# Performance work log

Hardware: AMD Instinct MI355X
Metric: run time of the kernel (lower is better)

The kernel has to match this reference:

```python
import jax, jax.numpy as jnp
import numpy as np

B, C, H, W = 8, 256, 128, 128
HEADS, DIM_HEAD = 4, 32
HID = HEADS * DIM_HEAD  # 128


def setup_inputs() -> dict:
    key = jax.random.key(0)
    k1, k2, k3, k4 = jax.random.split(key, 4)
    x = jax.random.normal(k1, (B, C, H, W), dtype=jnp.float32)
    # 1x1 conv weights stored as [out_ch, in_ch]
    w_qkv = jax.random.normal(k2, (3 * HID, C), dtype=jnp.float32) * (1.0 / np.sqrt(C))
    w_out = jax.random.normal(k3, (C, HID), dtype=jnp.float32) * (1.0 / np.sqrt(HID))
    b_out = jax.random.normal(k4, (C,), dtype=jnp.float32) * 0.01
    return {"x": x, "w_qkv": w_qkv, "w_out": w_out, "b_out": b_out}


def reference(x, w_qkv, w_out, b_out):
    b, c, h, w = x.shape
    n = h * w
    # 1x1 conv == channel matmul
    qkv = jnp.einsum('oc,bchw->bohw', w_qkv, x)  # [b, 3*HID, h, w]
    q, k, v = jnp.split(qkv, 3, axis=1)
    # rearrange 'b (heads d) h w -> b heads d (h w)'
    def to_heads(t):
        return t.reshape(b, HEADS, DIM_HEAD, n)
    q, k, v = to_heads(q), to_heads(k), to_heads(v)
    k = jax.nn.softmax(k, axis=-1)  # over spatial n
    # q_scale is False: q used as-is
    context = jnp.einsum('bhdn,bhen->bhde', k, v)   # [b, heads, d, e] small
    out = jnp.einsum('bhde,bhdn->bhen', context, q)  # [b, heads, e, n]
    out = out.reshape(b, HID, h, w)
    out = jnp.einsum('oc,bchw->bohw', w_out, out) + b_out[None, :, None, None]
    return out
```

## Files before the change

kernel.cpp:

```cpp
#include <hip/hip_runtime.h>
#include <stdint.h>

#define BB 8
#define CIN 256
#define NSP 16384
#define HID 128

typedef __bf16 bfrag __attribute__((ext_vector_type(8)));
typedef float  f32x4 __attribute__((ext_vector_type(4)));

__device__ __forceinline__ unsigned short f2bf(float f) {
  union { float f; unsigned int u; } v; v.f = f;
  unsigned int u = v.u;
  return (unsigned short)((u + 0x7FFFu + ((u >> 16) & 1u)) >> 16);
}

__global__ __launch_bounds__(256) void la_prep(const float* __restrict__ w_qkv,
                                               unsigned short* __restrict__ wkvb) {
  const int blk = blockIdx.x;
  const int t = threadIdx.x;
  const int off = (blk * 256 + t) * 4;
  const float4 wv4 = *(const float4*)(w_qkv + (size_t)128 * CIN + off);
  ushort4 p;
  p.x = f2bf(wv4.x); p.y = f2bf(wv4.y); p.z = f2bf(wv4.z); p.w = f2bf(wv4.w);
  *(ushort4*)(wkvb + off) = p;
}

__global__ __launch_bounds__(512, 4) void la_fused(const float* __restrict__ x,
                                                   const unsigned short* __restrict__ wkvb,
                                                   float* __restrict__ ctxp,
                                                   float* __restrict__ sumsp) {
  __shared__ __align__(16) union {
    struct { unsigned short Xb[2][128][40]; } g;
    struct { unsigned short Lk[64][140]; unsigned short Lv[64][140];
             float Pc[4][1024]; } e;
  } sh;
  const int chunk = blockIdx.x;
  const int n0 = chunk * 128;
  const int b = blockIdx.y;
  const int t = threadIdx.x;
  const int lane = t & 63, wv = t >> 6;
  const int l15 = lane & 15, q = lane >> 4;
  const int cl = t & 31;
  const int n16 = (t >> 5) * 8;
  const float* xp = x + (size_t)b * CIN * NSP + n0;
  f32x4 acc[2][8];
#pragma unroll
  for (int i = 0; i < 2; ++i)
#pragma unroll
    for (int j = 0; j < 8; ++j) acc[i][j] = 0.0f;

  float4 xa0, xa1;
  {
    const float* xr = xp + (size_t)cl * NSP + n16;
    xa0 = *(const float4*)xr;
    xa1 = *(const float4*)(xr + 4);
  }
  {
    sh.g.Xb[0][n16 + 0][cl] = f2bf(xa0.x);
    sh.g.Xb[0][n16 + 1][cl] = f2bf(xa0.y);
    sh.g.Xb[0][n16 + 2][cl] = f2bf(xa0.z);
    sh.g.Xb[0][n16 + 3][cl] = f2bf(xa0.w);
    sh.g.Xb[0][n16 + 4][cl] = f2bf(xa1.x);
    sh.g.Xb[0][n16 + 5][cl] = f2bf(xa1.y);
    sh.g.Xb[0][n16 + 6][cl] = f2bf(xa1.z);
    sh.g.Xb[0][n16 + 7][cl] = f2bf(xa1.w);
    const float* xr = xp + (size_t)(32 + cl) * NSP + n16;
    xa0 = *(const float4*)xr;
    xa1 = *(const float4*)(xr + 4);
  }
  __syncthreads();

#pragma unroll
  for (int kc = 0; kc < 8; ++kc) {
    const int p = kc & 1;
    bfrag a0 = *(const bfrag*)(wkvb + (size_t)(wv * 16 + l15) * CIN + kc * 32 + q * 8);
    bfrag a1 = *(const bfrag*)(wkvb + (size_t)(128 + wv * 16 + l15) * CIN + kc * 32 + q * 8);
    if (kc < 7) {
      sh.g.Xb[p ^ 1][n16 + 0][cl] = f2bf(xa0.x);
      sh.g.Xb[p ^ 1][n16 + 1][cl] = f2bf(xa0.y);
      sh.g.Xb[p ^ 1][n16 + 2][cl] = f2bf(xa0.z);
      sh.g.Xb[p ^ 1][n16 + 3][cl] = f2bf(xa0.w);
      sh.g.Xb[p ^ 1][n16 + 4][cl] = f2bf(xa1.x);
      sh.g.Xb[p ^ 1][n16 + 5][cl] = f2bf(xa1.y);
      sh.g.Xb[p ^ 1][n16 + 6][cl] = f2bf(xa1.z);
      sh.g.Xb[p ^ 1][n16 + 7][cl] = f2bf(xa1.w);
      if (kc < 6) {
        const float* xr = xp + (size_t)((kc + 2) * 32 + cl) * NSP + n16;
        xa0 = *(const float4*)xr;
        xa1 = *(const float4*)(xr + 4);
      }
    }
#pragma unroll
    for (int ni = 0; ni < 8; ++ni) {
      bfrag bbv = *(const bfrag*)&sh.g.Xb[p][ni * 16 + l15][q * 8];
      acc[0][ni] = __builtin_amdgcn_mfma_f32_16x16x32_bf16(a0, bbv, acc[0][ni], 0, 0, 0);
      acc[1][ni] = __builtin_amdgcn_mfma_f32_16x16x32_bf16(a1, bbv, acc[1][ni], 0, 0, 0);
    }
    __syncthreads();
  }

#pragma unroll
  for (int ni = 0; ni < 8; ++ni)
#pragma unroll
    for (int rg = 0; rg < 4; ++rg) acc[0][ni][rg] = __expf(acc[0][ni][rg]);

  {
    float sp[4] = {0.f, 0.f, 0.f, 0.f};
#pragma unroll
    for (int ni = 0; ni < 8; ++ni)
#pragma unroll
      for (int rg = 0; rg < 4; ++rg) sp[rg] += acc[0][ni][rg];
#pragma unroll
    for (int rg = 0; rg < 4; ++rg) {
      float s = sp[rg];
      s += __shfl_down(s, 8, 16);
      s += __shfl_down(s, 4, 16);
      s += __shfl_down(s, 2, 16);
      s += __shfl_down(s, 1, 16);
      if (l15 == 0)
        sumsp[((size_t)b * 128 + chunk) * 128 + wv * 16 + q * 4 + rg] = s;
    }
  }
  float* cp = ctxp + ((size_t)b * 128 + chunk) * 4096;
#pragma unroll
  for (int ph = 0; ph < 2; ++ph) {
    if ((wv >> 2) == ph) {
      const int r = (wv & 3) * 16 + q * 4;
#pragma unroll
      for (int ni = 0; ni < 8; ++ni)
#pragma unroll
        for (int rg = 0; rg < 4; ++rg) {
          sh.e.Lk[r + rg][ni * 16 + l15] = f2bf(acc[0][ni][rg]);
          sh.e.Lv[r + rg][ni * 16 + l15] = f2bf(acc[1][ni][rg]);
        }
    }
    __syncthreads();
    const int hl = wv >> 2, nq = wv & 3;
    f32x4 c2[2][2];
    c2[0][0] = 0.f; c2[0][1] = 0.f; c2[1][0] = 0.f; c2[1][1] = 0.f;
    bfrag ka[2], vb[2];
#pragma unroll
    for (int d2 = 0; d2 < 2; ++d2)
      ka[d2] = *(const bfrag*)&sh.e.Lk[hl * 32 + d2 * 16 + l15][nq * 32 + q * 8];
#pragma unroll
    for (int e2 = 0; e2 < 2; ++e2)
      vb[e2] = *(const bfrag*)&sh.e.Lv[hl * 32 + e2 * 16 + l15][nq * 32 + q * 8];
#pragma unroll
    for (int d2 = 0; d2 < 2; ++d2)
#pragma unroll
      for (int e2 = 0; e2 < 2; ++e2)
        c2[d2][e2] = __builtin_amdgcn_mfma_f32_16x16x32_bf16(ka[d2], vb[e2], c2[d2][e2], 0, 0, 0);
    const int slot = hl * 2 + (nq & 1);
    if (nq < 2) {
#pragma unroll
      for (int d2 = 0; d2 < 2; ++d2)
#pragma unroll
        for (int e2 = 0; e2 < 2; ++e2)
#pragma unroll
          for (int rg = 0; rg < 4; ++rg)
            sh.e.Pc[slot][(d2 * 16 + q * 4 + rg) * 32 + e2 * 16 + l15] = c2[d2][e2][rg];
    }
    __syncthreads();
    if (nq >= 2) {
#pragma unroll
      for (int d2 = 0; d2 < 2; ++d2)
#pragma unroll
        for (int e2 = 0; e2 < 2; ++e2)
#pragma unroll
          for (int rg = 0; rg < 4; ++rg)
            sh.e.Pc[slot][(d2 * 16 + q * 4 + rg) * 32 + e2 * 16 + l15] += c2[d2][e2][rg];
    }
    __syncthreads();
    for (int idx = t; idx < 2048; idx += 512) {
      const int h2 = idx >> 10, pos = idx & 1023;
      cp[(ph * 2 + h2) * 1024 + pos] = sh.e.Pc[h2 * 2][pos] + sh.e.Pc[h2 * 2 + 1][pos];
    }
    __syncthreads();
  }
}

__global__ __launch_bounds__(256) void la_reduce(const float* __restrict__ ctxp,
                                                 const float* __restrict__ sumsp,
                                                 float* __restrict__ ctxu,
                                                 float* __restrict__ sums) {
  const int blk = blockIdx.x;
  const int t = threadIdx.x;
  if (blk < 128) {
    const int gid = blk * 256 + t;
    const int b = gid >> 12, pos = gid & 4095;
    const float* base = ctxp + (size_t)b * 128 * 4096 + pos;
    float s = 0.f;
#pragma unroll 8
    for (int c = 0; c < 128; ++c) s += base[(size_t)c * 4096];
    ctxu[gid] = s;
  } else {
    const int gid = (blk - 128) * 256 + t;
    const int b = gid >> 7, row = gid & 127;
    const float* base = sumsp + (size_t)b * 128 * 128 + row;
    float s = 0.f;
#pragma unroll 8
    for (int c = 0; c < 128; ++c) s += base[c * 128];
    sums[gid] = s;
  }
}

__global__ __launch_bounds__(256) void la_mid(const float* __restrict__ w_out,
                                              const float* __restrict__ ctxu,
                                              const float* __restrict__ sums,
                                              const float* __restrict__ w_qkv,
                                              unsigned short* __restrict__ wcomb) {
  __shared__ float wrow[128];
  const int o = blockIdx.x;
  const int b = blockIdx.y;
  const int t = threadIdx.x;
  if (t < 128) {
    const int h = t >> 5, d = t & 31;
    const float* wr = w_out + (size_t)o * HID + h * 32;
    const float* cr = ctxu + ((size_t)(b * 4 + h) * 32 + d) * 32;
    float s = 0.f;
#pragma unroll 8
    for (int e = 0; e < 32; ++e) s += wr[e] * cr[e];
    wrow[t] = s * (1.0f / sums[b * 128 + t]);
  }
  __syncthreads();
  float s = 0.f;
#pragma unroll 8
  for (int hd = 0; hd < 128; ++hd) s += wrow[hd] * w_qkv[(size_t)hd * CIN + t];
  wcomb[((size_t)b * 256 + o) * 256 + t] = f2bf(s);
}

__global__ __launch_bounds__(512, 4) void la_out(const unsigned short* __restrict__ wcomb,
                                                 const float* __restrict__ x,
                                                 const float* __restrict__ b_out,
                                                 float* __restrict__ out) {
  __shared__ __align__(16) unsigned short Bt[2][128][40];
  const int n0 = blockIdx.x * 128;
  const int b = blockIdx.y;
  const int t = threadIdx.x;
  const int lane = t & 63, wv = t >> 6;
  const int l15 = lane & 15, q = lane >> 4;
  const int wm = (wv & 3) * 64;
  const int wn = (wv >> 2) * 64;
  const int cl = t & 31, n16 = (t >> 5) * 8;
  const float* xp = x + (size_t)b * CIN * NSP + n0;
  const unsigned short* abase = wcomb + (size_t)b * 256 * 256;
  f32x4 acc[4][4];
#pragma unroll
  for (int i = 0; i < 4; ++i)
#pragma unroll
    for (int j = 0; j < 4; ++j) acc[i][j] = 0.0f;

  float4 xa0, xa1;
  {
    const float* xr = xp + (size_t)cl * NSP + n16;
    xa0 = *(const float4*)xr;
    xa1 = *(const float4*)(xr + 4);
  }
  {
    Bt[0][n16 + 0][cl] = f2bf(xa0.x);
    Bt[0][n16 + 1][cl] = f2bf(xa0.y);
    Bt[0][n16 + 2][cl] = f2bf(xa0.z);
    Bt[0][n16 + 3][cl] = f2bf(xa0.w);
    Bt[0][n16 + 4][cl] = f2bf(xa1.x);
    Bt[0][n16 + 5][cl] = f2bf(xa1.y);
    Bt[0][n16 + 6][cl] = f2bf(xa1.z);
    Bt[0][n16 + 7][cl] = f2bf(xa1.w);
    const float* xr = xp + (size_t)(32 + cl) * NSP + n16;
    xa0 = *(const float4*)xr;
    xa1 = *(const float4*)(xr + 4);
  }
  __syncthreads();

#pragma unroll
  for (int kc = 0; kc < 8; ++kc) {
    const int p = kc & 1;
    bfrag a[4];
#pragma unroll
    for (int mi = 0; mi < 4; ++mi)
      a[mi] = *(const bfrag*)(abase + (size_t)(wm + mi * 16 + l15) * 256 + kc * 32 + q * 8);
    if (kc < 7) {
      Bt[p ^ 1][n16 + 0][cl] = f2bf(xa0.x);
      Bt[p ^ 1][n16 + 1][cl] = f2bf(xa0.y);
      Bt[p ^ 1][n16 + 2][cl] = f2bf(xa0.z);
      Bt[p ^ 1][n16 + 3][cl] = f2bf(xa0.w);
      Bt[p ^ 1][n16 + 4][cl] = f2bf(xa1.x);
      Bt[p ^ 1][n16 + 5][cl] = f2bf(xa1.y);
      Bt[p ^ 1][n16 + 6][cl] = f2bf(xa1.z);
      Bt[p ^ 1][n16 + 7][cl] = f2bf(xa1.w);
      if (kc < 6) {
        const float* xr = xp + (size_t)((kc + 2) * 32 + cl) * NSP + n16;
        xa0 = *(const float4*)xr;
        xa1 = *(const float4*)(xr + 4);
      }
    }
#pragma unroll
    for (int ni = 0; ni < 4; ++ni) {
      bfrag bbv = *(const bfrag*)&Bt[p][wn + ni * 16 + l15][q * 8];
#pragma unroll
      for (int mi = 0; mi < 4; ++mi)
        acc[mi][ni] = __builtin_amdgcn_mfma_f32_16x16x32_bf16(a[mi], bbv, acc[mi][ni], 0, 0, 0);
    }
    __syncthreads();
  }
  float* obase = out + (size_t)b * 256 * NSP;
#pragma unroll
  for (int mi = 0; mi < 4; ++mi) {
    const int ob = wm + mi * 16 + q * 4;
    const float4 bias = *(const float4*)(b_out + ob);
    float ba[4] = {bias.x, bias.y, bias.z, bias.w};
#pragma unroll
    for (int ni = 0; ni < 4; ++ni) {
      const int n = n0 + wn + ni * 16 + l15;
#pragma unroll
      for (int rg = 0; rg < 4; ++rg)
        obase[(size_t)(ob + rg) * NSP + n] = acc[mi][ni][rg] + ba[rg];
    }
  }
}


extern "C" void kernel_launch(void* const* d_in, const int* in_sizes, int n_in,
                              void* d_out, int out_size, void* d_ws, size_t ws_size,
                              hipStream_t stream) {
  (void)in_sizes; (void)n_in; (void)out_size; (void)ws_size;
  const float* x     = (const float*)d_in[0];
  const float* w_qkv = (const float*)d_in[1];
  const float* w_out = (const float*)d_in[2];
  const float* b_out = (const float*)d_in[3];
  float* out = (float*)d_out;
  char* ws = (char*)d_ws;
  unsigned short* wkvb  = (unsigned short*)(ws);
  float* ctxp           = (float*)(ws + 131072);
  float* sumsp          = (float*)(ws + 16908288);
  float* ctxu           = (float*)(ws + 17432576);
  float* sums           = (float*)(ws + 17563648);
  unsigned short* wcomb = (unsigned short*)(ws + 17567744);

  la_prep<<<dim3(64), dim3(256), 0, stream>>>(w_qkv, wkvb);
  la_fused<<<dim3(NSP / 128, BB), dim3(512), 0, stream>>>(x, wkvb, ctxp, sumsp);
  la_reduce<<<dim3(132), dim3(256), 0, stream>>>(ctxp, sumsp, ctxu, sums);
  la_mid<<<dim3(256, BB), dim3(256), 0, stream>>>(w_out, ctxu, sums, w_qkv, wcomb);
  la_out<<<dim3(NSP / 128, BB), dim3(512), 0, stream>>>(wcomb, x, b_out, out);
}
```

Before: 319.4 us.

## Write bf16 transposed x from fused kernel and reuse it in output GEMM

The first fused GEMM kernel now also writes its bf16-converted, transposed x tile to a workspace buffer. The output GEMM reads those bf16 fragments directly from global memory instead of rereading fp32 x, converting it and staging it through LDS with barriers. This removes conversion, LDS traffic and syncs from the output kernel. In exchange the first kernel gains extra global stores and the workspace grows.

```diff
diff --git a/kernel.cpp b/kernel.cpp
--- a/kernel.cpp
+++ b/kernel.cpp
@@ -8,6 +8,7 @@
 
 typedef __bf16 bfrag __attribute__((ext_vector_type(8)));
 typedef float  f32x4 __attribute__((ext_vector_type(4)));
+typedef unsigned short us8 __attribute__((ext_vector_type(8)));
 
 __device__ __forceinline__ unsigned short f2bf(float f) {
   union { float f; unsigned int u; } v; v.f = f;
@@ -28,6 +29,7 @@
 
 __global__ __launch_bounds__(512, 4) void la_fused(const float* __restrict__ x,
                                                    const unsigned short* __restrict__ wkvb,
+                                                   unsigned short* __restrict__ xT,
                                                    float* __restrict__ ctxp,
                                                    float* __restrict__ sumsp) {
   __shared__ __align__(16) union {
@@ -44,6 +46,7 @@
   const int cl = t & 31;
   const int n16 = (t >> 5) * 8;
   const float* xp = x + (size_t)b * CIN * NSP + n0;
+  unsigned short* xTb = xT + ((size_t)b * NSP + n0) * CIN;
   f32x4 acc[2][8];
 #pragma unroll
   for (int i = 0; i < 2; ++i)
@@ -91,6 +94,11 @@
         xa1 = *(const float4*)(xr + 4);
       }
     }
+    {
+      const int rr = t >> 2, cc8 = (t & 3) * 8;
+      const us8 wb = *(const us8*)&sh.g.Xb[p][rr][cc8];
+      *(us8*)(xTb + (size_t)rr * CIN + kc * 32 + cc8) = wb;
+    }
 #pragma unroll
     for (int ni = 0; ni < 8; ++ni) {
       bfrag bbv = *(const bfrag*)&sh.g.Xb[p][ni * 16 + l15][q * 8];
@@ -231,10 +239,9 @@
 }
 
 __global__ __launch_bounds__(512, 4) void la_out(const unsigned short* __restrict__ wcomb,
-                                                 const float* __restrict__ x,
+                                                 const unsigned short* __restrict__ xT,
                                                  const float* __restrict__ b_out,
                                                  float* __restrict__ out) {
-  __shared__ __align__(16) unsigned short Bt[2][128][40];
   const int n0 = blockIdx.x * 128;
   const int b = blockIdx.y;
   const int t = threadIdx.x;
@@ -242,66 +249,28 @@
   const int l15 = lane & 15, q = lane >> 4;
   const int wm = (wv & 3) * 64;
   const int wn = (wv >> 2) * 64;
-  const int cl = t & 31, n16 = (t >> 5) * 8;
-  const float* xp = x + (size_t)b * CIN * NSP + n0;
   const unsigned short* abase = wcomb + (size_t)b * 256 * 256;
+  const unsigned short* xb = xT + ((size_t)b * NSP + n0) * CIN;
   f32x4 acc[4][4];
 #pragma unroll
   for (int i = 0; i < 4; ++i)
 #pragma unroll
     for (int j = 0; j < 4; ++j) acc[i][j] = 0.0f;
 
-  float4 xa0, xa1;
-  {
-    const float* xr = xp + (size_t)cl * NSP + n16;
-    xa0 = *(const float4*)xr;
-    xa1 = *(const float4*)(xr + 4);
-  }
-  {
-    Bt[0][n16 + 0][cl] = f2bf(xa0.x);
-    Bt[0][n16 + 1][cl] = f2bf(xa0.y);
-    Bt[0][n16 + 2][cl] = f2bf(xa0.z);
-    Bt[0][n16 + 3][cl] = f2bf(xa0.w);
-    Bt[0][n16 + 4][cl] = f2bf(xa1.x);
-    Bt[0][n16 + 5][cl] = f2bf(xa1.y);
-    Bt[0][n16 + 6][cl] = f2bf(xa1.z);
-    Bt[0][n16 + 7][cl] = f2bf(xa1.w);
-    const float* xr = xp + (size_t)(32 + cl) * NSP + n16;
-    xa0 = *(const float4*)xr;
-    xa1 = *(const float4*)(xr + 4);
-  }
-  __syncthreads();
-
 #pragma unroll
   for (int kc = 0; kc < 8; ++kc) {
-    const int p = kc & 1;
-    bfrag a[4];
+    bfrag a[4], bv[4];
 #pragma unroll
     for (int mi = 0; mi < 4; ++mi)
       a[mi] = *(const bfrag*)(abase + (size_t)(wm + mi * 16 + l15) * 256 + kc * 32 + q * 8);
-    if (kc < 7) {
-      Bt[p ^ 1][n16 + 0][cl] = f2bf(xa0.x);
-      Bt[p ^ 1][n16 + 1][cl] = f2bf(xa0.y);
-      Bt[p ^ 1][n16 + 2][cl] = f2bf(xa0.z);
-      Bt[p ^ 1][n16 + 3][cl] = f2bf(xa0.w);
-      Bt[p ^ 1][n16 + 4][cl] = f2bf(xa1.x);
-      Bt[p ^ 1][n16 + 5][cl] = f2bf(xa1.y);
-      Bt[p ^ 1][n16 + 6][cl] = f2bf(xa1.z);
-      Bt[p ^ 1][n16 + 7][cl] = f2bf(xa1.w);
-      if (kc < 6) {
-        const float* xr = xp + (size_t)((kc + 2) * 32 + cl) * NSP + n16;
-        xa0 = *(const float4*)xr;
-        xa1 = *(const float4*)(xr + 4);
-      }
-    }
-#pragma unroll
-    for (int ni = 0; ni < 4; ++ni) {
-      bfrag bbv = *(const bfrag*)&Bt[p][wn + ni * 16 + l15][q * 8];
+#pragma unroll
+    for (int ni = 0; ni < 4; ++ni)
+      bv[ni] = *(const bfrag*)(xb + (size_t)(wn + ni * 16 + l15) * CIN + kc * 32 + q * 8);
+#pragma unroll
+    for (int ni = 0; ni < 4; ++ni)
 #pragma unroll
       for (int mi = 0; mi < 4; ++mi)
-        acc[mi][ni] = __builtin_amdgcn_mfma_f32_16x16x32_bf16(a[mi], bbv, acc[mi][ni], 0, 0, 0);
-    }
-    __syncthreads();
+        acc[mi][ni] = __builtin_amdgcn_mfma_f32_16x16x32_bf16(a[mi], bv[ni], acc[mi][ni], 0, 0, 0);
   }
   float* obase = out + (size_t)b * 256 * NSP;
 #pragma unroll
@@ -331,15 +300,16 @@
   float* out = (float*)d_out;
   char* ws = (char*)d_ws;
   unsigned short* wkvb  = (unsigned short*)(ws);
-  float* ctxp           = (float*)(ws + 131072);
-  float* sumsp          = (float*)(ws + 16908288);
-  float* ctxu           = (float*)(ws + 17432576);
-  float* sums           = (float*)(ws + 17563648);
-  unsigned short* wcomb = (unsigned short*)(ws + 17567744);
+  unsigned short* xTws  = (unsigned short*)(ws + 131072);
+  float* ctxp           = (float*)(ws + 67239936);
+  float* sumsp          = (float*)(ws + 84017152);
+  float* ctxu           = (float*)(ws + 84541440);
+  float* sums           = (float*)(ws + 84672512);
+  unsigned short* wcomb = (unsigned short*)(ws + 84676608);
 
   la_prep<<<dim3(64), dim3(256), 0, stream>>>(w_qkv, wkvb);
-  la_fused<<<dim3(NSP / 128, BB), dim3(512), 0, stream>>>(x, wkvb, ctxp, sumsp);
+  la_fused<<<dim3(NSP / 128, BB), dim3(512), 0, stream>>>(x, wkvb, xTws, ctxp, sumsp);
   la_reduce<<<dim3(132), dim3(256), 0, stream>>>(ctxp, sumsp, ctxu, sums);
   la_mid<<<dim3(256, BB), dim3(256), 0, stream>>>(w_out, ctxu, sums, w_qkv, wcomb);
-  la_out<<<dim3(NSP / 128, BB), dim3(512), 0, stream>>>(wcomb, x, b_out, out);
-}
+  la_out<<<dim3(NSP / 128, BB), dim3(512), 0, stream>>>(wcomb, xTws, b_out, out);
+}
```

Result: slower. 350.6 us (+9.8%).
